# Performance work log

Measured on AMD Instinct MI355X. Metric: run time of the kernel, lower is better.

The kernel has to match this reference:

```python
import jax, jax.numpy as jnp
import numpy as np

STATE = 256
IN = 128
OUT = 128


def setup_inputs() -> dict:
    key = jax.random.key(0)
    ks = jax.random.split(key, 10)
    u = jax.random.normal(ks[0], (8, 2048, IN), dtype=jnp.float32)
    x0_re = jax.random.normal(ks[1], (8, STATE), dtype=jnp.float32)
    x0_im = jax.random.normal(ks[2], (8, STATE), dtype=jnp.float32)
    # A init: 2*pi*rand angles on unit circle, scaled by 10 (enforce_stability=True)
    theta = 2.0 * jnp.pi * jax.random.uniform(ks[3], (STATE,), dtype=jnp.float32)
    A_re = 10.0 * jnp.cos(theta)
    A_im = 10.0 * jnp.sin(theta)
    # complex randn: real/imag parts each have variance 1/2
    inv_sqrt2 = 1.0 / np.sqrt(2.0)
    sB = inv_sqrt2 / np.sqrt(STATE + IN)
    B_re = jax.random.normal(ks[4], (IN, STATE), dtype=jnp.float32) * sB
    B_im = jax.random.normal(ks[5], (IN, STATE), dtype=jnp.float32) * sB
    sC = inv_sqrt2 / np.sqrt(STATE + OUT)
    C_re = jax.random.normal(ks[6], (STATE, OUT), dtype=jnp.float32) * sC
    C_im = jax.random.normal(ks[7], (STATE, OUT), dtype=jnp.float32) * sC
    D = jnp.zeros((IN, OUT), dtype=jnp.float32)
    b = jnp.zeros((OUT,), dtype=jnp.float32)
    return {"u": u, "x0_re": x0_re, "x0_im": x0_im, "A_re": A_re, "A_im": A_im,
            "B_re": B_re, "B_im": B_im, "C_re": C_re, "C_im": C_im, "D": D, "b": b}


def reference(u, x0_re, x0_im, A_re, A_im, B_re, B_im, C_re, C_im, D, b):
    cdt = jnp.complex64
    length = u.shape[1]
    A = (A_re + 1j * A_im).astype(cdt)
    # enforce_stability: map poles inside unit disc
    A = A / jnp.sqrt(A * jnp.conj(A) + 1.0)
    # Vandermonde powers A^t for t in [0, length]  -> [length+1, n]
    Aps = A[None, :] ** jnp.arange(length + 1)[:, None]
    Bm = (B_re + 1j * B_im).astype(cdt)
    uB = u.astype(cdt) @ Bm  # [batch, length, n]
    # FFT-based causal convolution of Aps[:-1] ([length, n]) with uB
    T = 2 ** int(np.ceil(np.log2(2 * length - 1)))
    AF = jnp.fft.fft(Aps[:-1], n=T, axis=0)      # [T, n]
    UF = jnp.fft.fft(uB, n=T, axis=1)            # [batch, T, n]
    x = jnp.fft.ifft(AF[None] * UF, axis=1)[:, :length]  # [batch, length, n]
    # add initial-state contribution A^t * x0
    x0 = (x0_re + 1j * x0_im).astype(cdt)
    x = x + Aps[1:][None] * x0[:, None, :]
    Cm = (C_re + 1j * C_im).astype(cdt)
    y = jnp.real(x @ Cm) + u @ D + b
    return y, x[:, -1]
```

## Files before the change

kernel.cpp:

```cpp
#include <hip/hip_runtime.h>
#include <math.h>

#define BATCH 8
#define T 2048
#define N 256
#define INF 128
#define OUTF 128
#define L 16
#define LOG2L 4
#define NC (T / L)
#define KTOT 640
#define NKS 20
#define NKU 4
#define ASTRIDE 40
#define UBS 516

typedef __attribute__((ext_vector_type(8))) short short8;
typedef __attribute__((ext_vector_type(4))) float f32x4;

__device__ __forceinline__ unsigned short f2b(float f) {
    union { float f; unsigned u; } x; x.f = f;
    unsigned r = (x.u + 0x7FFFu + ((x.u >> 16) & 1u)) >> 16;
    return (unsigned short)r;
}
__device__ __forceinline__ float b2f(unsigned short s) {
    union { unsigned u; float f; } x; x.u = ((unsigned)s) << 16;
    return x.f;
}

__global__ __launch_bounds__(256) void k_prep(const float* __restrict__ Are,
                                              const float* __restrict__ Aim,
                                              const float* __restrict__ Bre,
                                              const float* __restrict__ Bim,
                                              const float* __restrict__ Cre,
                                              const float* __restrict__ Cim,
                                              const float* __restrict__ D,
                                              float2* __restrict__ Apow,
                                              unsigned short* __restrict__ Bswz,
                                              unsigned short* __restrict__ Bswz2) {
    int blk = blockIdx.x;
    int tid = threadIdx.x;
    if (blk < 40) {
        int unit = blk * 4 + (tid >> 6);
        int ks = unit >> 3, ot = unit & 7;
        int l = tid & 63;
        int o = ot * 16 + (l & 15);
        int k0 = ks * 32 + (l >> 4) * 8;
        short8 out;
#pragma unroll
        for (int j = 0; j < 8; ++j) {
            int gk = k0 + j;
            float v = (gk < 256) ? Cre[gk * OUTF + o]
                    : (gk < 512) ? -Cim[(gk - 256) * OUTF + o]
                                 : D[(gk - 512) * OUTF + o];
            out[j] = (short)f2b(v);
        }
        *(short8*)(Bswz + ((size_t)unit * 64 + l) * 8) = out;
    } else if (blk < 72) {
        int unit = (blk - 40) * 4 + (tid >> 6);
        int l = tid & 63;
        int col = (unit & 31) * 16 + (l & 15);
        int k0 = (unit >> 5) * 32 + (l >> 4) * 8;
        short8 out;
#pragma unroll
        for (int j = 0; j < 8; ++j) {
            int gk = k0 + j;
            float v = (col < 256) ? Bre[gk * N + col] : Bim[gk * N + col - 256];
            out[j] = (short)f2b(v);
        }
        *(short8*)(Bswz2 + ((size_t)unit * 64 + l) * 8) = out;
    } else {
        int n = tid;
        float ar = Are[n], ai = Aim[n];
        float inv = 1.0f / sqrtf(ar * ar + ai * ai + 1.0f);
        ar *= inv; ai *= inv;
        float pr = ar, pi = ai;
        for (int j = 0; j < L; ++j) {
            Apow[j * N + n] = make_float2(pr, pi);
            float nr = pr * ar - pi * ai;
            float ni = pr * ai + pi * ar;
            pr = nr; pi = ni;
        }
    }
}

__global__ __launch_bounds__(512, 2) void kU_scan(const float* __restrict__ u,
                                                  const unsigned short* __restrict__ Bswz2,
                                                  const float2* __restrict__ Apow,
                                                  unsigned short* __restrict__ xbb,
                                                  float2* __restrict__ carr) {
    __shared__ float uB[32][UBS];
    int tid = threadIdx.x;
    int lane = tid & 63;
    int w = tid >> 6;
    int rg = w >> 2;
    int cq = w & 3;
    size_t row0 = (size_t)blockIdx.x * 32;
    const float* uprow = u + (row0 + rg * 16 + (lane & 15)) * INF + (lane >> 4) * 8;

    f32x4 acc[8];
#pragma unroll
    for (int i = 0; i < 8; ++i) acc[i] = (f32x4){0.f, 0.f, 0.f, 0.f};

    const short8* Bfr2 = (const short8*)Bswz2;
#pragma unroll
    for (int ks = 0; ks < NKU; ++ks) {
        float4 a0 = *(const float4*)(uprow + ks * 32);
        float4 a1 = *(const float4*)(uprow + ks * 32 + 4);
        short8 af;
        af[0] = (short)f2b(a0.x); af[1] = (short)f2b(a0.y);
        af[2] = (short)f2b(a0.z); af[3] = (short)f2b(a0.w);
        af[4] = (short)f2b(a1.x); af[5] = (short)f2b(a1.y);
        af[6] = (short)f2b(a1.z); af[7] = (short)f2b(a1.w);
#pragma unroll
        for (int i = 0; i < 8; ++i) {
            int ct = cq * 8 + i;
            short8 bf = Bfr2[(size_t)(ks * 32 + ct) * 64 + lane];
            acc[i] = __builtin_amdgcn_mfma_f32_16x16x32_bf16(af, bf, acc[i], 0, 0, 0);
        }
    }
    {
        int rbase = rg * 16 + (lane >> 4) * 4;
        int cb = lane & 15;
#pragma unroll
        for (int i = 0; i < 8; ++i) {
            int col = (cq * 8 + i) * 16 + cb;
#pragma unroll
            for (int r = 0; r < 4; ++r)
                uB[rbase + r][col] = acc[i][r];
        }
    }
    __syncthreads();

    int ch = tid >> 8;
    int n = tid & 255;
    size_t rowg0 = row0 + ch * 16;
    int b = (int)(rowg0 >> 11);
    int c = (int)((rowg0 & 2047) >> LOG2L);
    float2 a = Apow[n];
    float xr = 0.f, xi = 0.f;
#pragma unroll
    for (int j = 0; j < 16; ++j) {
        float ur = uB[ch * 16 + j][n];
        float ui = uB[ch * 16 + j][256 + n];
        float nr = fmaf(a.x, xr, fmaf(-a.y, xi, ur));
        float ni = fmaf(a.x, xi, fmaf(a.y, xr, ui));
        xr = nr; xi = ni;
        size_t rowg = rowg0 + j;
        xbb[rowg * 512 + n]       = f2b(xr);
        xbb[rowg * 512 + 256 + n] = f2b(xi);
    }
    carr[((size_t)b * NC + c) * N + n] = make_float2(xr, xi);
}

__global__ __launch_bounds__(256) void k2_carry(const float* __restrict__ x0re,
                                                const float* __restrict__ x0im,
                                                const float2* __restrict__ Apow,
                                                float2* __restrict__ carr,
                                                float* __restrict__ out_tail,
                                                int tail_mode) {
    int b = blockIdx.x, n = threadIdx.x;
    float pr = x0re[b * N + n], pi = x0im[b * N + n];
    float2 aL = Apow[(L - 1) * N + n];
#pragma unroll 8
    for (int c = 0; c < NC; ++c) {
        size_t off = ((size_t)b * NC + c) * N + n;
        float2 f = carr[off];
        carr[off] = make_float2(pr, pi);
        float nr = f.x + aL.x * pr - aL.y * pi;
        float ni = f.y + aL.x * pi + aL.y * pr;
        pr = nr; pi = ni;
    }
    if (tail_mode == 2) {
        out_tail[(b * N + n) * 2 + 0] = pr;
        out_tail[(b * N + n) * 2 + 1] = pi;
    } else if (tail_mode == 1) {
        out_tail[b * N + n] = pr;
    }
}

__global__ __launch_bounds__(256) void k3_mfma(const unsigned short* __restrict__ xbb,
                                               const float2* __restrict__ Apow,
                                               const float2* __restrict__ carr,
                                               const float* __restrict__ u,
                                               const unsigned short* __restrict__ Bswz,
                                               const float* __restrict__ bias,
                                               float* __restrict__ y) {
    __shared__ unsigned short As[64 * ASTRIDE];
    int tid = threadIdx.x;
    int lane = tid & 63;
    int w = tid >> 6;

    int srow = tid >> 2;
    int kq = (tid & 3) * 8;
    size_t rowg = (size_t)blockIdx.x * 64 + srow;
    int b = (int)(rowg >> 11);
    int t = (int)(rowg & 2047);
    int jrow = t & (L - 1);
    int crow = t >> LOG2L;
    const float4* Ap4 = (const float4*)Apow;
    const float4* Cv4 = (const float4*)carr;
    size_t apbase = ((size_t)jrow * N) >> 1;
    size_t cvbase = (((size_t)b * NC + crow) * N) >> 1;

    f32x4 acc[8];
#pragma unroll
    for (int ot = 0; ot < 8; ++ot) acc[ot] = (f32x4){0.f, 0.f, 0.f, 0.f};

    float4 pa[4], pv[4], pu0, pu1;
    short8 pxb;

    auto LOAD = [&](int ks) {
        if (ks < 16) {
            int n0 = (ks & 7) * 32 + kq;
            int col0 = ((ks < 8) ? 0 : 256) + n0;
            pxb = *(const short8*)(xbb + rowg * 512 + col0);
#pragma unroll
            for (int q = 0; q < 4; ++q) {
                pa[q] = Ap4[apbase + (n0 >> 1) + q];
                pv[q] = Cv4[cvbase + (n0 >> 1) + q];
            }
        } else {
            const float4* up = (const float4*)(u + rowg * INF + (ks - 16) * 32 + kq);
            pu0 = up[0]; pu1 = up[1];
        }
    };
    auto WRITE = [&](int ks) {
        short8 st;
        if (ks < 16) {
#pragma unroll
            for (int j = 0; j < 8; ++j) {
                float xv = b2f((unsigned short)pxb[j]);
                float4 aq = pa[j >> 1];
                float4 vq = pv[j >> 1];
                float px = (j & 1) ? aq.z : aq.x;
                float py = (j & 1) ? aq.w : aq.y;
                float vx = (j & 1) ? vq.z : vq.x;
                float vy = (j & 1) ? vq.w : vq.y;
                float corr = (ks < 8) ? (px * vx - py * vy) : (px * vy + py * vx);
                st[j] = (short)f2b(xv + corr);
            }
        } else {
#pragma unroll
            for (int j = 0; j < 8; ++j) {
                float uv = (j < 4) ? ((j == 0) ? pu0.x : (j == 1) ? pu0.y : (j == 2) ? pu0.z : pu0.w)
                                   : ((j == 4) ? pu1.x : (j == 5) ? pu1.y : (j == 6) ? pu1.z : pu1.w);
                st[j] = (short)f2b(uv);
            }
        }
        *(short8*)(&As[srow * ASTRIDE + kq]) = st;
    };

    const short8* Bfr = (const short8*)Bswz;
    const short8* afp = (const short8*)&As[(w * 16 + (lane & 15)) * ASTRIDE + (lane >> 4) * 8];

    LOAD(0);
    for (int ks = 0; ks < NKS; ++ks) {
        WRITE(ks);
        __syncthreads();
        if (ks < NKS - 1) LOAD(ks + 1);
        short8 af = *afp;
#pragma unroll
        for (int ot = 0; ot < 8; ++ot) {
            short8 bf = Bfr[((size_t)ks * 8 + ot) * 64 + lane];
            acc[ot] = __builtin_amdgcn_mfma_f32_16x16x32_bf16(af, bf, acc[ot], 0, 0, 0);
        }
        __syncthreads();
    }

    int colb = lane & 15;
    int rq = lane >> 4;
#pragma unroll
    for (int ot = 0; ot < 8; ++ot) {
        int o = ot * 16 + colb;
        float bv = bias[o];
#pragma unroll
        for (int r = 0; r < 4; ++r) {
            int row = w * 16 + rq * 4 + r;
            y[((size_t)blockIdx.x * 64 + row) * OUTF + o] = acc[ot][r] + bv;
        }
    }
}

extern "C" void kernel_launch(void* const* d_in, const int* in_sizes, int n_in,
                              void* d_out, int out_size, void* d_ws, size_t ws_size,
                              hipStream_t stream) {
    const float* u    = (const float*)d_in[0];
    const float* x0re = (const float*)d_in[1];
    const float* x0im = (const float*)d_in[2];
    const float* Are  = (const float*)d_in[3];
    const float* Aim  = (const float*)d_in[4];
    const float* Bre  = (const float*)d_in[5];
    const float* Bim  = (const float*)d_in[6];
    const float* Cre  = (const float*)d_in[7];
    const float* Cim  = (const float*)d_in[8];
    const float* D    = (const float*)d_in[9];
    const float* bias = (const float*)d_in[10];
    float* y = (float*)d_out;

    char* ws = (char*)d_ws;
    float2* Apow = (float2*)ws;
    char* p = ws + (size_t)L * N * sizeof(float2);
    float2* carr = (float2*)p;
    p += (size_t)BATCH * NC * N * sizeof(float2);
    unsigned short* xbb = (unsigned short*)p;
    p += (size_t)BATCH * T * 512 * sizeof(unsigned short);
    unsigned short* Bswz = (unsigned short*)p;
    p += (size_t)NKS * 8 * 64 * 8 * sizeof(unsigned short);
    unsigned short* Bswz2 = (unsigned short*)p;

    const int ysz = BATCH * T * OUTF;
    const int tail_elems = out_size - ysz;
    int tail_mode = (tail_elems >= BATCH * N * 2) ? 2
                  : (tail_elems >= BATCH * N) ? 1 : 0;
    float* tail = y + ysz;

    k_prep<<<73, 256, 0, stream>>>(Are, Aim, Bre, Bim, Cre, Cim, D, Apow, Bswz, Bswz2);
    kU_scan<<<(BATCH * T) / 32, 512, 0, stream>>>(u, Bswz2, Apow, xbb, carr);
    k2_carry<<<BATCH, 256, 0, stream>>>(x0re, x0im, Apow, carr, tail, tail_mode);
    k3_mfma<<<(BATCH * T) / 64, 256, 0, stream>>>(xbb, Apow, carr, u, Bswz, bias, y);
}
```

Before: 61.06 us.

## Split carry correction into separate kernel and load MFMA A-operands directly from global

Result: slower. 76.70 us (+25.6%).

```diff
diff --git a/kernel.cpp b/kernel.cpp
--- a/kernel.cpp
+++ b/kernel.cpp
@@ -12,7 +12,6 @@
 #define KTOT 640
 #define NKS 20
 #define NKU 4
-#define ASTRIDE 40
 #define UBS 516
 
 typedef __attribute__((ext_vector_type(8))) short short8;
@@ -179,105 +178,94 @@
     }
 }
 
+__global__ __launch_bounds__(256) void k2b_corr(const float2* __restrict__ Apow,
+                                                const float2* __restrict__ carr,
+                                                unsigned short* __restrict__ xbb) {
+    int c = blockIdx.x, b = blockIdx.y;
+    int tid = threadIdx.x;
+    const float4* Ap4 = (const float4*)Apow;
+    const float4* Cv4 = (const float4*)(carr + ((size_t)b * NC + c) * N);
+    size_t rowbase = ((size_t)b * T + (size_t)c * L) * 512;
+
+#pragma unroll
+    for (int i = 0; i < 4; ++i) {
+        int unit = tid + i * 256;
+        int j = unit >> 6;
+        int g = unit & 63;
+        int re = (g < 32);
+        int n0 = (g & 31) * 8;
+        unsigned short* px = xbb + rowbase + (size_t)j * 512 + g * 8;
+        short8 xv = *(const short8*)px;
+        float4 ap[4], vv[4];
+#pragma unroll
+        for (int q = 0; q < 4; ++q) {
+            ap[q] = Ap4[((size_t)j * N + n0) / 2 + q];
+            vv[q] = Cv4[n0 / 2 + q];
+        }
+        short8 st;
+#pragma unroll
+        for (int e = 0; e < 8; ++e) {
+            float4 aq = ap[e >> 1];
+            float4 vq = vv[e >> 1];
+            float pr = (e & 1) ? aq.z : aq.x;
+            float pi = (e & 1) ? aq.w : aq.y;
+            float vr = (e & 1) ? vq.z : vq.x;
+            float vi = (e & 1) ? vq.w : vq.y;
+            float corr = re ? (pr * vr - pi * vi) : (pr * vi + pi * vr);
+            st[e] = (short)f2b(b2f((unsigned short)xv[e]) + corr);
+        }
+        *(short8*)px = st;
+    }
+}
+
 __global__ __launch_bounds__(256) void k3_mfma(const unsigned short* __restrict__ xbb,
-                                               const float2* __restrict__ Apow,
-                                               const float2* __restrict__ carr,
                                                const float* __restrict__ u,
                                                const unsigned short* __restrict__ Bswz,
                                                const float* __restrict__ bias,
                                                float* __restrict__ y) {
-    __shared__ unsigned short As[64 * ASTRIDE];
     int tid = threadIdx.x;
     int lane = tid & 63;
     int w = tid >> 6;
-
-    int srow = tid >> 2;
-    int kq = (tid & 3) * 8;
-    size_t rowg = (size_t)blockIdx.x * 64 + srow;
-    int b = (int)(rowg >> 11);
-    int t = (int)(rowg & 2047);
-    int jrow = t & (L - 1);
-    int crow = t >> LOG2L;
-    const float4* Ap4 = (const float4*)Apow;
-    const float4* Cv4 = (const float4*)carr;
-    size_t apbase = ((size_t)jrow * N) >> 1;
-    size_t cvbase = (((size_t)b * NC + crow) * N) >> 1;
+    size_t rowg = (size_t)blockIdx.x * 64 + w * 16 + (lane & 15);
+    int koff = (lane >> 4) * 8;
+    const unsigned short* arow = xbb + rowg * 512 + koff;
+    const float* urow = u + rowg * INF + koff;
+    const short8* Bfr = (const short8*)Bswz;
 
     f32x4 acc[8];
 #pragma unroll
     for (int ot = 0; ot < 8; ++ot) acc[ot] = (f32x4){0.f, 0.f, 0.f, 0.f};
 
-    float4 pa[4], pv[4], pu0, pu1;
-    short8 pxb;
-
-    auto LOAD = [&](int ks) {
+#pragma unroll 4
+    for (int ks = 0; ks < NKS; ++ks) {
+        short8 af;
         if (ks < 16) {
-            int n0 = (ks & 7) * 32 + kq;
-            int col0 = ((ks < 8) ? 0 : 256) + n0;
-            pxb = *(const short8*)(xbb + rowg * 512 + col0);
-#pragma unroll
-            for (int q = 0; q < 4; ++q) {
-                pa[q] = Ap4[apbase + (n0 >> 1) + q];
-                pv[q] = Cv4[cvbase + (n0 >> 1) + q];
-            }
+            af = *(const short8*)(arow + ks * 32);
         } else {
-            const float4* up = (const float4*)(u + rowg * INF + (ks - 16) * 32 + kq);
-            pu0 = up[0]; pu1 = up[1];
-        }
-    };
-    auto WRITE = [&](int ks) {
-        short8 st;
-        if (ks < 16) {
-#pragma unroll
-            for (int j = 0; j < 8; ++j) {
-                float xv = b2f((unsigned short)pxb[j]);
-                float4 aq = pa[j >> 1];
-                float4 vq = pv[j >> 1];
-                float px = (j & 1) ? aq.z : aq.x;
-                float py = (j & 1) ? aq.w : aq.y;
-                float vx = (j & 1) ? vq.z : vq.x;
-                float vy = (j & 1) ? vq.w : vq.y;
-                float corr = (ks < 8) ? (px * vx - py * vy) : (px * vy + py * vx);
-                st[j] = (short)f2b(xv + corr);
-            }
-        } else {
-#pragma unroll
-            for (int j = 0; j < 8; ++j) {
-                float uv = (j < 4) ? ((j == 0) ? pu0.x : (j == 1) ? pu0.y : (j == 2) ? pu0.z : pu0.w)
-                                   : ((j == 4) ? pu1.x : (j == 5) ? pu1.y : (j == 6) ? pu1.z : pu1.w);
-                st[j] = (short)f2b(uv);
-            }
-        }
-        *(short8*)(&As[srow * ASTRIDE + kq]) = st;
-    };
-
-    const short8* Bfr = (const short8*)Bswz;
-    const short8* afp = (const short8*)&As[(w * 16 + (lane & 15)) * ASTRIDE + (lane >> 4) * 8];
-
-    LOAD(0);
-    for (int ks = 0; ks < NKS; ++ks) {
-        WRITE(ks);
-        __syncthreads();
-        if (ks < NKS - 1) LOAD(ks + 1);
-        short8 af = *afp;
+            float4 a0 = *(const float4*)(urow + (ks - 16) * 32);
+            float4 a1 = *(const float4*)(urow + (ks - 16) * 32 + 4);
+            af[0] = (short)f2b(a0.x); af[1] = (short)f2b(a0.y);
+            af[2] = (short)f2b(a0.z); af[3] = (short)f2b(a0.w);
+            af[4] = (short)f2b(a1.x); af[5] = (short)f2b(a1.y);
+            af[6] = (short)f2b(a1.z); af[7] = (short)f2b(a1.w);
+        }
 #pragma unroll
         for (int ot = 0; ot < 8; ++ot) {
             short8 bf = Bfr[((size_t)ks * 8 + ot) * 64 + lane];
             acc[ot] = __builtin_amdgcn_mfma_f32_16x16x32_bf16(af, bf, acc[ot], 0, 0, 0);
         }
-        __syncthreads();
     }
 
     int colb = lane & 15;
     int rq = lane >> 4;
+    size_t rowout = (size_t)blockIdx.x * 64 + w * 16 + rq * 4;
 #pragma unroll
     for (int ot = 0; ot < 8; ++ot) {
         int o = ot * 16 + colb;
         float bv = bias[o];
 #pragma unroll
         for (int r = 0; r < 4; ++r) {
-            int row = w * 16 + rq * 4 + r;
-            y[((size_t)blockIdx.x * 64 + row) * OUTF + o] = acc[ot][r] + bv;
+            y[(rowout + r) * OUTF + o] = acc[ot][r] + bv;
         }
     }
 }
@@ -318,5 +306,6 @@
     k_prep<<<73, 256, 0, stream>>>(Are, Aim, Bre, Bim, Cre, Cim, D, Apow, Bswz, Bswz2);
     kU_scan<<<(BATCH * T) / 32, 512, 0, stream>>>(u, Bswz2, Apow, xbb, carr);
     k2_carry<<<BATCH, 256, 0, stream>>>(x0re, x0im, Apow, carr, tail, tail_mode);
-    k3_mfma<<<(BATCH * T) / 64, 256, 0, stream>>>(xbb, Apow, carr, u, Bswz, bias, y);
-}
+    k2b_corr<<<dim3(NC, BATCH), 256, 0, stream>>>(Apow, carr, xbb);
+    k3_mfma<<<(BATCH * T) / 64, 256, 0, stream>>>(xbb, u, Bswz, bias, y);
+}
```
